# Kernel optimization log

Hardware: AMD Instinct MI355X
Metric: run time of the kernel (lower is better)

The kernel has to match this reference:

```python
import jax, jax.numpy as jnp
import numpy as np
import math

MAXL = 3
TAUS = [16, 16, 16, 16]
OUT_TAUS = [16, 16, 16, 16]
BM_CNT = 1.0
BM_EPS = 1e-5

# (l1, l2, l) triples in the kernel's triple-loop order, bucketed by output l
TRIPLES = {l: [] for l in range(MAXL + 1)}
for _l1 in range(MAXL + 1):
    for _l2 in range(_l1 + 1):
        for _l in range(_l1 - _l2, min(_l1 + _l2, MAXL) + 1):
            TRIPLES[_l].append((_l1, _l2))

MIDDLE_TAUS = [sum(TAUS[a] * TAUS[b] for (a, b) in TRIPLES[l]) for l in range(MAXL + 1)]


def _cg_coef(l1, m1, l2, m2, l, m):
    if m1 + m2 != m:
        return 0.0
    f = math.factorial
    pre = math.sqrt((2 * l + 1) * f(l1 + l2 - l) * f(l1 - l2 + l) * f(-l1 + l2 + l) / f(l1 + l2 + l + 1))
    pre *= math.sqrt(f(l + m) * f(l - m) * f(l1 - m1) * f(l1 + m1) * f(l2 - m2) * f(l2 + m2))
    s = 0.0
    for k in range(0, l1 + l2 - l + 1):
        d = [k, l1 + l2 - l - k, l1 - m1 - k, l2 + m2 - k, l - l2 + m1 + k, l - l1 - m2 + k]
        if any(x < 0 for x in d):
            continue
        den = 1.0
        for x in d:
            den *= f(x)
        s += (-1.0) ** k / den
    return pre * s


def _cg_tensor(l1, l2, l):
    t = np.zeros((2 * l1 + 1, 2 * l2 + 1, 2 * l + 1), dtype=np.float32)
    for i, m1 in enumerate(range(-l1, l1 + 1)):
        for j, m2 in enumerate(range(-l2, l2 + 1)):
            m = m1 + m2
            if -l <= m <= l:
                t[i, j, m + l] = _cg_coef(l1, m1, l2, m2, l, m)
    return t

CG = {}
for _l in range(MAXL + 1):
    for (_l1, _l2) in TRIPLES[_l]:
        CG[(_l1, _l2, _l)] = jnp.asarray(_cg_tensor(_l1, _l2, _l))

# complex-multiply contraction tensor: (a*b)[k] = a[i] b[j] CM[i,j,k]
_CM = np.zeros((2, 2, 2), dtype=np.float32)
_CM[0, 0, 0] = 1.0; _CM[1, 1, 0] = -1.0; _CM[0, 1, 1] = 1.0; _CM[1, 0, 1] = 1.0
CM = jnp.asarray(_CM)


def setup_inputs() -> dict:
    key = jax.random.key(0)
    k1, k2, k3 = jax.random.split(key, 3)
    in_len = sum(TAUS[l] * (2 * l + 1) for l in range(MAXL + 1))  # 256
    wlen = sum(OUT_TAUS[l] * MIDDLE_TAUS[l] for l in range(MAXL + 1))  # 90112
    activations = jax.random.normal(k1, (2048, in_len, 2), dtype=jnp.float32)
    W = 0.05 * jax.random.uniform(k2, (wlen, 2), dtype=jnp.float32)
    bn_stds = jax.random.uniform(k3, (sum(MIDDLE_TAUS),), dtype=jnp.float32)
    return {"activations": activations, "W": W, "bn_stds": bn_stds}


def reference(activations, W, bn_stds):
    B = activations.shape[0]
    # split input into per-l parts: [B, tau_l, 2l+1, 2]
    Fs = []
    st = 0
    for l in range(MAXL + 1):
        ln = TAUS[l] * (2 * l + 1)
        Fs.append(activations[:, st:st + ln, :].reshape(B, TAUS[l], 2 * l + 1, 2))
        st += ln
    outs = []
    w_st = 0
    s_st = 0
    for l in range(MAXL + 1):
        # Clebsch-Gordan products feeding output degree l
        mids = []
        for (l1, l2) in TRIPLES[l]:
            c = jnp.einsum('btmi,bsnj,mnp,ijk->btspk', Fs[l1], Fs[l2], CG[(l1, l2, l)], CM)
            mids.append(c.reshape(B, TAUS[l1] * TAUS[l2], 2 * l + 1, 2))
        mid = jnp.concatenate(mids, axis=1)  # [B, M_l, 2l+1, 2]
        Ml = MIDDLE_TAUS[l]
        # fused batchnorm: per-middle-channel std over batch and m, moving average update
        batch_std = jnp.sqrt(jnp.mean(jnp.sum(mid * mid, axis=-1), axis=(0, 2)))  # [M_l]
        mov = bn_stds[s_st:s_st + Ml]
        new_std = (mov * BM_CNT + batch_std) / (BM_CNT + 1.0)
        mid = mid / (new_std + BM_EPS)[None, :, None, None]
        # complex linear mix over middle channels -> out_taus[l]
        wl = jax.lax.dynamic_slice_in_dim(W, w_st, OUT_TAUS[l] * Ml, axis=0).reshape(OUT_TAUS[l], Ml, 2)
        out_l = jnp.einsum('oci,bcmj,ijk->bomk', wl, mid, CM)
        outs.append(out_l.reshape(B, OUT_TAUS[l] * (2 * l + 1), 2))
        w_st += OUT_TAUS[l] * Ml
        s_st += Ml
    return jnp.concatenate(outs, axis=1)  # [B, 256, 2]
```

## Files before the change

### kernel.cpp

```cpp
#include <hip/hip_runtime.h>
#include <math.h>

typedef __attribute__((ext_vector_type(8))) short bf16x8;
typedef __attribute__((ext_vector_type(4))) float f32x4;

constexpr double cfact(int n){ double r=1.0; for(int i=2;i<=n;++i) r*=(double)i; return r; }
constexpr double csqrt_(double x){ double g=(x>1.0)?x:1.0; for(int i=0;i<100;++i) g=0.5*(g+x/g); return g; }
constexpr double cg_coef_(int l1,int m1,int l2,int m2,int l,int m){
  double pre = csqrt_((double)(2*l+1)*cfact(l1+l2-l)*cfact(l1-l2+l)*cfact(-l1+l2+l)/cfact(l1+l2+l+1));
  pre = pre*csqrt_(cfact(l+m)*cfact(l-m)*cfact(l1-m1)*cfact(l1+m1)*cfact(l2-m2)*cfact(l2+m2));
  double s=0.0;
  for(int k=0;k<=l1+l2-l;++k){
    int d0=k,d1=l1+l2-l-k,d2=l1-m1-k,d3=l2+m2-k,d4=l-l2+m1+k,d5=l-l1-m2+k;
    if(d0<0||d1<0||d2<0||d3<0||d4<0||d5<0) continue;
    double den=cfact(d0)*cfact(d1)*cfact(d2)*cfact(d3)*cfact(d4)*cfact(d5);
    s+=((k&1)?-1.0:1.0)/den;
  }
  return pre*s;
}
struct CGList{ int n; float coef[64]; int mi[64]; int ni[64]; int pi[64]; };
constexpr CGList build_cg(int l1,int l2,int l){
  CGList T{};
  for(int i=0;i<2*l1+1;++i){
    for(int j=0;j<2*l2+1;++j){
      int m1=i-l1, m2=j-l2, m=m1+m2;
      if(m<-l||m>l) continue;
      double c=cg_coef_(l1,m1,l2,m2,l,m);
      if(c>1e-12||c<-1e-12){
        T.coef[T.n]=(float)c; T.mi[T.n]=i; T.ni[T.n]=j; T.pi[T.n]=m+l; T.n++;
      }
    }
  }
  return T;
}

__device__ __host__ constexpr int AOFF(int l){ return l==0?0: l==1?16: l==2?64:144; }
__device__ __host__ constexpr int MLs(int l){ return l==0?1024: l==1?1536: l==2?1792:1536; }
__device__ __host__ constexpr int WOFF(int l){ return l==0?0: l==1?16384: l==2?40960:69632; }
__device__ __host__ constexpr int SOFF(int l){ return l==0?0: l==1?1024: l==2?2560:4352; }
__device__ __host__ constexpr int NTRI(int l){ return l==0?4: l==1?6: l==2?7:6; }
__device__ __host__ constexpr int ABASE(int l){ return l==0?0: l==1?65536: l==2?163840:278528; }
__device__ __host__ constexpr size_t MBW(int l){ return l==0?0 : l==1?2097152 : l==2?11534336 : 29884416; }
#define MID_OFF 1048576
#define MID_BYTES ((size_t)51904512*4)

#define DEVFN __device__ __forceinline__
#define LPITCH 144
#define APITCH 132

DEVFN unsigned f2bf2(float x, float y){
  unsigned ux = __float_as_uint(x); ux = (ux + 0x7FFFu + ((ux>>16)&1u)) >> 16;
  unsigned uy = __float_as_uint(y); uy = (uy + 0x7FFFu + ((uy>>16)&1u)) >> 16;
  return (ux & 0xFFFFu) | (uy << 16);
}

template<int L1,int L2,int L>
DEVFN void cg_accum(const float2* F1, const float2* F2, float2* mid){
  constexpr CGList T = build_cg(L1,L2,L);
  #pragma unroll
  for(int e=0;e<T.n;++e){
    const float c = T.coef[e];
    const float2 a = F1[T.mi[e]];
    const float2 b = F2[T.ni[e]];
    float pr = a.x*b.x - a.y*b.y;
    float pim= a.x*b.y + a.y*b.x;
    mid[T.pi[e]].x += c*pr;
    mid[T.pi[e]].y += c*pim;
  }
}

template<int L1,int L2,int L,int Q>
DEVFN void k1_body(const float2* __restrict__ acts, int b0, int u, int bh,
                   float& ssa, float& ssb, unsigned* __restrict__ midw){
  constexpr int N1=2*L1+1, N2=2*L2+1, NP=2*L+1, Ml=MLs(L);
  const int t = u>>3, s0 = (u&7)*2;
  unsigned* midq = midw ? (midw + MBW(L) + (size_t)Q*256) : nullptr;
  #pragma unroll 2
  for(int bi=0;bi<8;++bi){
    const int row = bh*8 + bi;
    const float2* arow = acts + row*256;
    float2 F1[N1], F2a[N2], F2b[N2], mida[NP], midb[NP];
    #pragma unroll
    for(int m=0;m<N1;++m) F1[m]=arow[AOFF(L1)+t*N1+m];
    #pragma unroll
    for(int n=0;n<N2;++n){
      F2a[n]=arow[AOFF(L2)+s0*N2+n];
      F2b[n]=arow[AOFF(L2)+(s0+1)*N2+n];
    }
    #pragma unroll
    for(int p=0;p<NP;++p){ mida[p]=make_float2(0.f,0.f); midb[p]=make_float2(0.f,0.f); }
    cg_accum<L1,L2,L>(F1,F2a,mida);
    cg_accum<L1,L2,L>(F1,F2b,midb);
    #pragma unroll
    for(int p=0;p<NP;++p){
      ssa += mida[p].x*mida[p].x + mida[p].y*mida[p].y;
      ssb += midb[p].x*midb[p].x + midb[p].y*midb[p].y;
    }
    if(midq){
      const size_t nrow = (size_t)(b0+row)*NP;
      #pragma unroll
      for(int p=0;p<NP;++p){
        uint2 v; v.x = f2bf2(mida[p].x, mida[p].y); v.y = f2bf2(midb[p].x, midb[p].y);
        ((uint2*)(midq + (nrow+p)*Ml))[u] = v;
      }
    }
  }
}

__global__ __launch_bounds__(256) void k_sumsq(const float* __restrict__ act,
                                               float* __restrict__ sumsq,
                                               unsigned* __restrict__ midw){
  __shared__ float2 acts[16*256];
  int bid=blockIdx.x;
  const int order[23] = {22,16,21,18,15,20,13,9,14,8,17,7,12,6,10,3,5,19,2,11,1,4,0};
  int ti = order[bid>>7];
  int b0 = (bid&127)*16;
  const int tid = threadIdx.x;
  {
    const float4* ag = (const float4*)act + (size_t)b0*128;
    float4* as4 = (float4*)acts;
    #pragma unroll
    for(int j=0;j<8;++j) as4[j*256+tid] = ag[j*256+tid];
  }
  __syncthreads();
  const int u = tid & 127, bh = tid >> 7;
  float ssa=0.f, ssb=0.f;
  switch(ti){
    case 0:  k1_body<0,0,0,0>(acts,b0,u,bh,ssa,ssb,midw); break;
    case 1:  k1_body<1,1,0,1>(acts,b0,u,bh,ssa,ssb,midw); break;
    case 2:  k1_body<2,2,0,2>(acts,b0,u,bh,ssa,ssb,midw); break;
    case 3:  k1_body<3,3,0,3>(acts,b0,u,bh,ssa,ssb,midw); break;
    case 4:  k1_body<1,0,1,0>(acts,b0,u,bh,ssa,ssb,midw); break;
    case 5:  k1_body<1,1,1,1>(acts,b0,u,bh,ssa,ssb,midw); break;
    case 6:  k1_body<2,1,1,2>(acts,b0,u,bh,ssa,ssb,midw); break;
    case 7:  k1_body<2,2,1,3>(acts,b0,u,bh,ssa,ssb,midw); break;
    case 8:  k1_body<3,2,1,4>(acts,b0,u,bh,ssa,ssb,midw); break;
    case 9:  k1_body<3,3,1,5>(acts,b0,u,bh,ssa,ssb,midw); break;
    case 10: k1_body<1,1,2,0>(acts,b0,u,bh,ssa,ssb,midw); break;
    case 11: k1_body<2,0,2,1>(acts,b0,u,bh,ssa,ssb,midw); break;
    case 12: k1_body<2,1,2,2>(acts,b0,u,bh,ssa,ssb,midw); break;
    case 13: k1_body<2,2,2,3>(acts,b0,u,bh,ssa,ssb,midw); break;
    case 14: k1_body<3,1,2,4>(acts,b0,u,bh,ssa,ssb,midw); break;
    case 15: k1_body<3,2,2,5>(acts,b0,u,bh,ssa,ssb,midw); break;
    case 16: k1_body<3,3,2,6>(acts,b0,u,bh,ssa,ssb,midw); break;
    case 17: k1_body<2,1,3,0>(acts,b0,u,bh,ssa,ssb,midw); break;
    case 18: k1_body<2,2,3,1>(acts,b0,u,bh,ssa,ssb,midw); break;
    case 19: k1_body<3,0,3,2>(acts,b0,u,bh,ssa,ssb,midw); break;
    case 20: k1_body<3,1,3,3>(acts,b0,u,bh,ssa,ssb,midw); break;
    case 21: k1_body<3,2,3,4>(acts,b0,u,bh,ssa,ssb,midw); break;
    default: k1_body<3,3,3,5>(acts,b0,u,bh,ssa,ssb,midw); break;
  }
  atomicAdd(&sumsq[ti*256 + 2*u],     ssa);
  atomicAdd(&sumsq[ti*256 + 2*u + 1], ssb);
}

__global__ __launch_bounds__(256) void k_buildA(const float* __restrict__ W,
                                                const float* __restrict__ bn,
                                                const float* __restrict__ sumsq,
                                                short* __restrict__ A){
  int idx = blockIdx.x*256 + threadIdx.x;
  if(idx>=5888) return;
  int l = (idx<1024)?0 : (idx<2560)?1 : (idx<4352)?2 : 3;
  float divi = (l==0)?(1.f/2048.f) : (l==1)?(1.f/6144.f) : (l==2)?(1.f/10240.f) : (1.f/14336.f);
  float bstd = sqrtf(sumsq[idx]*divi);
  float nstd = 0.5f*(bn[idx]+bstd);
  float s = 1.f/(nstd+1e-5f);
  int c = idx - SOFF(l);
  int Ml = MLs(l);
  const float2* wbase = (const float2*)W + WOFF(l) + c;
  unsigned* Aw = (unsigned*)(A + ABASE(l));
  for(int o=0;o<16;++o){
    float2 w = wbase[(size_t)o*Ml];
    Aw[(size_t)o*Ml + c]      = f2bf2(w.x*s, -w.y*s);
    Aw[(size_t)(o+16)*Ml + c] = f2bf2(w.y*s,  w.x*s);
  }
}

template<int L>
DEVFN void k4_panel(int tg, const unsigned* __restrict__ midl,
                    const short* __restrict__ A_l, float* __restrict__ out,
                    unsigned* ldsA){
  constexpr int NP = 2*L+1;
  constexpr int Ml = MLs(L);
  constexpr int NK = Ml/16;
  constexpr int P  = NK/8;
  const int tid = threadIdx.x;
  const int lane = tid & 63, w = tid >> 6;
  const int col = lane & 15, quad = lane >> 4;
  const int nt = tg*8 + w;
  const unsigned* Aw = (const unsigned*)A_l;
  const unsigned* bp = midl + (size_t)(nt*16 + col)*Ml + quad*4;

  const int r0 = tid >> 5,        j0 = (tid & 31)*4;
  const int r1 = (tid+512) >> 5,  j1 = j0;

  f32x4 cR = {0.f,0.f,0.f,0.f};
  f32x4 cI = {0.f,0.f,0.f,0.f};
  {
    uint4 v0 = *(const uint4*)(Aw + (size_t)r0*Ml + j0);
    uint4 v1 = *(const uint4*)(Aw + (size_t)r1*Ml + j1);
    *(uint4*)(ldsA + r0*APITCH + j0) = v0;
    *(uint4*)(ldsA + r1*APITCH + j1) = v1;
  }
  __syncthreads();
  for(int p=0; p<P; ++p){
    const unsigned* buf  = ldsA + (p&1)*(32*APITCH);
    unsigned* nbuf = ldsA + ((p+1)&1)*(32*APITCH);
    uint4 v0, v1;
    if(p+1 < P){
      v0 = *(const uint4*)(Aw + (size_t)r0*Ml + (p+1)*128 + j0);
      v1 = *(const uint4*)(Aw + (size_t)r1*Ml + (p+1)*128 + j1);
    }
    const unsigned* bpp = bp + p*128;
    const unsigned* a0 = buf + col*APITCH + quad*4;
    const unsigned* a1 = buf + (col+16)*APITCH + quad*4;
    #pragma unroll
    for(int c=0; c<8; ++c){
      bf16x8 b  = *(const bf16x8*)(bpp + c*16);
      bf16x8 A0 = *(const bf16x8*)(a0 + c*16);
      bf16x8 A1 = *(const bf16x8*)(a1 + c*16);
      cR = __builtin_amdgcn_mfma_f32_16x16x32_bf16(A0, b, cR, 0, 0, 0);
      cI = __builtin_amdgcn_mfma_f32_16x16x32_bf16(A1, b, cI, 0, 0, 0);
    }
    if(p+1 < P){
      *(uint4*)(nbuf + r0*APITCH + j0) = v0;
      *(uint4*)(nbuf + r1*APITCH + j1) = v1;
    }
    __syncthreads();
  }
  const int n = nt*16 + col;
  const int b = n / NP, pp = n % NP;
  float2* out2 = (float2*)out;
  #pragma unroll
  for(int i=0;i<4;++i){
    const int o = quad*4 + i;
    out2[(size_t)b*256 + AOFF(L) + o*NP + pp] = make_float2(cR[i], cI[i]);
  }
}

__global__ __launch_bounds__(512) void k_gemm4(const unsigned* __restrict__ midw,
                                               const short* __restrict__ A,
                                               float* __restrict__ out){
  __shared__ unsigned ldsA[2*32*APITCH];
  const int bid = blockIdx.x;
  if(bid < 16)       k4_panel<0>(bid,       midw+MBW(0), A+ABASE(0), out, ldsA);
  else if(bid < 64)  k4_panel<1>(bid - 16,  midw+MBW(1), A+ABASE(1), out, ldsA);
  else if(bid < 144) k4_panel<2>(bid - 64,  midw+MBW(2), A+ABASE(2), out, ldsA);
  else               k4_panel<3>(bid - 144, midw+MBW(3), A+ABASE(3), out, ldsA);
}

template<int L1,int L2,int L>
DEVFN void phase1(const float2* __restrict__ act2, unsigned* ldsw,
                  int half, int c0, int bh4, int b_lo, int b_hi, int n0){
  constexpr int N1=2*L1+1, N2=2*L2+1, NP=2*L+1;
  const int s  = c0 & 15;
  const int t1 = half*8 + (c0>>4);
  const int t2 = t1 + 4;
  for(int b = b_lo + bh4; b <= b_hi; b += 4){
    const float2* arow = act2 + (size_t)b*256;
    float2 F1a[N1], F1b[N1], F2[N2], mida[NP], midb[NP];
    #pragma unroll
    for(int m=0;m<N1;++m){
      F1a[m]=arow[AOFF(L1)+t1*N1+m];
      F1b[m]=arow[AOFF(L1)+t2*N1+m];
    }
    #pragma unroll
    for(int n=0;n<N2;++n) F2[n]=arow[AOFF(L2)+s*N2+n];
    #pragma unroll
    for(int p=0;p<NP;++p){ mida[p]=make_float2(0.f,0.f); midb[p]=make_float2(0.f,0.f); }
    cg_accum<L1,L2,L>(F1a,F2,mida);
    cg_accum<L1,L2,L>(F1b,F2,midb);
    int nb = b*NP - n0;
    #pragma unroll
    for(int p=0;p<NP;++p){
      int n = nb + p;
      if(n>=0 && n<32){
        ldsw[n*LPITCH + c0]      = f2bf2(mida[p].x, mida[p].y);
        ldsw[n*LPITCH + c0 + 64] = f2bf2(midb[p].x, midb[p].y);
      }
    }
  }
}

template<int L>
DEVFN void p1_dispatch(int q, int half, const float2* __restrict__ act2, unsigned* ldsw,
                       int c0,int bh4,int b_lo,int b_hi,int n0){
  if constexpr(L==0){
    switch(q){
      case 0: phase1<0,0,0>(act2,ldsw,half,c0,bh4,b_lo,b_hi,n0); break;
      case 1: phase1<1,1,0>(act2,ldsw,half,c0,bh4,b_lo,b_hi,n0); break;
      case 2: phase1<2,2,0>(act2,ldsw,half,c0,bh4,b_lo,b_hi,n0); break;
      default:phase1<3,3,0>(act2,ldsw,half,c0,bh4,b_lo,b_hi,n0); break;
    }
  } else if constexpr(L==1){
    switch(q){
      case 0: phase1<1,0,1>(act2,ldsw,half,c0,bh4,b_lo,b_hi,n0); break;
      case 1: phase1<1,1,1>(act2,ldsw,half,c0,bh4,b_lo,b_hi,n0); break;
      case 2: phase1<2,1,1>(act2,ldsw,half,c0,bh4,b_lo,b_hi,n0); break;
      case 3: phase1<2,2,1>(act2,ldsw,half,c0,bh4,b_lo,b_hi,n0); break;
      case 4: phase1<3,2,1>(act2,ldsw,half,c0,bh4,b_lo,b_hi,n0); break;
      default:phase1<3,3,1>(act2,ldsw,half,c0,bh4,b_lo,b_hi,n0); break;
    }
  } else if constexpr(L==2){
    switch(q){
      case 0: phase1<1,1,2>(act2,ldsw,half,c0,bh4,b_lo,b_hi,n0); break;
      case 1: phase1<2,0,2>(act2,ldsw,half,c0,bh4,b_lo,b_hi,n0); break;
      case 2: phase1<2,1,2>(act2,ldsw,half,c0,bh4,b_lo,b_hi,n0); break;
      case 3: phase1<2,2,2>(act2,ldsw,half,c0,bh4,b_lo,b_hi,n0); break;
      case 4: phase1<3,1,2>(act2,ldsw,half,c0,bh4,b_lo,b_hi,n0); break;
      case 5: phase1<3,2,2>(act2,ldsw,half,c0,bh4,b_lo,b_hi,n0); break;
      default:phase1<3,3,2>(act2,ldsw,half,c0,bh4,b_lo,b_hi,n0); break;
    }
  } else {
    switch(q){
      case 0: phase1<2,1,3>(act2,ldsw,half,c0,bh4,b_lo,b_hi,n0); break;
      case 1: phase1<2,2,3>(act2,ldsw,half,c0,bh4,b_lo,b_hi,n0); break;
      case 2: phase1<3,0,3>(act2,ldsw,half,c0,bh4,b_lo,b_hi,n0); break;
      case 3: phase1<3,1,3>(act2,ldsw,half,c0,bh4,b_lo,b_hi,n0); break;
      case 4: phase1<3,2,3>(act2,ldsw,half,c0,bh4,b_lo,b_hi,n0); break;
      default:phase1<3,3,3>(act2,ldsw,half,c0,bh4,b_lo,b_hi,n0); break;
    }
  }
}

template<int L>
DEVFN void k3_gemm(int n0, const float2* __restrict__ act2,
                   const short* __restrict__ A_l, float* __restrict__ out,
                   unsigned* lds){
  constexpr int NP = 2*L+1;
  constexpr int NT = NTRI(L);
  constexpr int pitchA = 2*MLs(L);
  const int tid = threadIdx.x;
  const int lane = tid & 63, wsub = tid >> 6;
  const int col = lane & 15, quad = lane >> 4;
  const int nh = wsub & 1, mh = wsub >> 1;
  const int c0 = tid & 63, bh4 = tid >> 6;
  const int b_lo = n0 / NP;
  const int b_hi = (n0 + 31) / NP;

  f32x4 acc = {0.f,0.f,0.f,0.f};
  const short* Ar = A_l + (size_t)(col + mh*16) * pitchA + quad*8;
  const int lds_rd = (nh*16 + col)*LPITCH + quad*4;

  for(int chunk = 0; chunk < 2*NT; ++chunk){
    const int q = chunk >> 1, half = chunk & 1;
    unsigned* buf = lds + (chunk & 1)*(32*LPITCH);
    p1_dispatch<L>(q, half, act2, buf, c0, bh4, b_lo, b_hi, n0);
    __syncthreads();
    const int kbase = q*512 + half*256;
    const char* ldsb = (const char*)(buf + lds_rd);
    #pragma unroll
    for(int ks=0; ks<8; ++ks){
      bf16x8 a = *(const bf16x8*)(Ar + kbase + ks*32);
      bf16x8 b = *(const bf16x8*)(ldsb + ks*64);
      acc = __builtin_amdgcn_mfma_f32_16x16x32_bf16(a, b, acc, 0, 0, 0);
    }
  }
  const int n = n0 + nh*16 + col;
  const int b = n / NP, p = n % NP;
  #pragma unroll
  for(int i=0;i<4;++i){
    const int o = quad*4 + i;
    out[((size_t)b*256 + AOFF(L) + o*NP + p)*2 + mh] = acc[i];
  }
}

__global__ __launch_bounds__(256) void k_gemm(const float* __restrict__ act,
                                              const short* __restrict__ A,
                                              float* __restrict__ out){
  __shared__ unsigned lds[2*32*LPITCH];
  const int bid = blockIdx.x;
  const float2* act2 = (const float2*)act;
  if(bid < 64)       k3_gemm<0>((bid      )*32, act2, A + ABASE(0), out, lds);
  else if(bid < 256) k3_gemm<1>((bid - 64 )*32, act2, A + ABASE(1), out, lds);
  else if(bid < 576) k3_gemm<2>((bid - 256)*32, act2, A + ABASE(2), out, lds);
  else               k3_gemm<3>((bid - 576)*32, act2, A + ABASE(3), out, lds);
}

extern "C" void kernel_launch(void* const* d_in, const int* in_sizes, int n_in,
                              void* d_out, int out_size, void* d_ws, size_t ws_size,
                              hipStream_t stream) {
  const float* act = (const float*)d_in[0];
  const float* W   = (const float*)d_in[1];
  const float* bn  = (const float*)d_in[2];
  float* out = (float*)d_out;

  float* sumsq = (float*)d_ws;
  short* A     = (short*)((char*)d_ws + 24576);
  const size_t REQ = (size_t)MID_OFF + MID_BYTES;
  unsigned* midw = (ws_size >= REQ) ? (unsigned*)((char*)d_ws + MID_OFF) : nullptr;

  hipMemsetAsync(sumsq, 0, 5888*sizeof(float), stream);
  hipLaunchKernelGGL(k_sumsq,  dim3(23*128), dim3(256), 0, stream, act, sumsq, midw);
  hipLaunchKernelGGL(k_buildA, dim3(23),     dim3(256), 0, stream, W, bn, sumsq, A);
  if(midw)
    hipLaunchKernelGGL(k_gemm4, dim3(256),  dim3(512), 0, stream, (const unsigned*)midw, A, out);
  else
    hipLaunchKernelGGL(k_gemm,  dim3(1024), dim3(256), 0, stream, act, A, out);
}
```

Baseline: 166.5 us.

## Register-prefetch B panels in GEMM, halve block size, use nontemporal mid stores

The final GEMM kernel now runs 256-thread blocks with 4 waves each, so there are twice as many blocks covering the same tiles. It double-buffers the bf16 middle-activation B operand in registers via nontemporal loads, one K-panel ahead, on top of the existing LDS double-buffer for A. The sumsq kernel now writes the intermediate mid tensor with nontemporal 64-bit stores to limit cache pollution. The aim is to hide global-load latency of the streamed B operand and improve occupancy and load balance. The costs are higher register pressure from holding 16 bf16x8 vectors, and the A panel is now reloaded by more blocks.

```diff
diff --git a/kernel.cpp b/kernel.cpp
--- a/kernel.cpp
+++ b/kernel.cpp
@@ -100,8 +100,10 @@
       const size_t nrow = (size_t)(b0+row)*NP;
       #pragma unroll
       for(int p=0;p<NP;++p){
-        uint2 v; v.x = f2bf2(mida[p].x, mida[p].y); v.y = f2bf2(midb[p].x, midb[p].y);
-        ((uint2*)(midq + (nrow+p)*Ml))[u] = v;
+        unsigned lo = f2bf2(mida[p].x, mida[p].y);
+        unsigned hi = f2bf2(midb[p].x, midb[p].y);
+        unsigned long long pv = (unsigned long long)lo | ((unsigned long long)hi<<32);
+        __builtin_nontemporal_store(pv, (unsigned long long*)(midq + (nrow+p)*Ml) + u);
       }
     }
   }
@@ -177,7 +179,7 @@
 }
 
 template<int L>
-DEVFN void k4_panel(int tg, const unsigned* __restrict__ midl,
+DEVFN void k5_panel(int tg, const unsigned* __restrict__ midl,
                     const short* __restrict__ A_l, float* __restrict__ out,
                     unsigned* ldsA){
   constexpr int NP = 2*L+1;
@@ -187,44 +189,57 @@
   const int tid = threadIdx.x;
   const int lane = tid & 63, w = tid >> 6;
   const int col = lane & 15, quad = lane >> 4;
-  const int nt = tg*8 + w;
+  const int nt = tg*4 + w;
   const unsigned* Aw = (const unsigned*)A_l;
   const unsigned* bp = midl + (size_t)(nt*16 + col)*Ml + quad*4;
 
-  const int r0 = tid >> 5,        j0 = (tid & 31)*4;
-  const int r1 = (tid+512) >> 5,  j1 = j0;
-
   f32x4 cR = {0.f,0.f,0.f,0.f};
   f32x4 cI = {0.f,0.f,0.f,0.f};
-  {
-    uint4 v0 = *(const uint4*)(Aw + (size_t)r0*Ml + j0);
-    uint4 v1 = *(const uint4*)(Aw + (size_t)r1*Ml + j1);
-    *(uint4*)(ldsA + r0*APITCH + j0) = v0;
-    *(uint4*)(ldsA + r1*APITCH + j1) = v1;
-  }
+
+  #pragma unroll
+  for(int sub=0;sub<4;++sub){
+    int idx = sub*256 + tid, r = idx>>5, j = (idx&31)*4;
+    *(uint4*)(ldsA + r*APITCH + j) = *(const uint4*)(Aw + (size_t)r*Ml + j);
+  }
+  bf16x8 b0[8], b1[8];
+  #pragma unroll
+  for(int c=0;c<8;++c) b0[c] = __builtin_nontemporal_load((const bf16x8*)(bp + c*16));
   __syncthreads();
-  for(int p=0; p<P; ++p){
-    const unsigned* buf  = ldsA + (p&1)*(32*APITCH);
-    unsigned* nbuf = ldsA + ((p+1)&1)*(32*APITCH);
-    uint4 v0, v1;
+
+  #pragma unroll
+  for(int p=0;p<P;++p){
+    bf16x8* bc = (p&1)? b1 : b0;
+    bf16x8* bn = (p&1)? b0 : b1;
     if(p+1 < P){
-      v0 = *(const uint4*)(Aw + (size_t)r0*Ml + (p+1)*128 + j0);
-      v1 = *(const uint4*)(Aw + (size_t)r1*Ml + (p+1)*128 + j1);
-    }
-    const unsigned* bpp = bp + p*128;
+      #pragma unroll
+      for(int c=0;c<8;++c)
+        bn[c] = __builtin_nontemporal_load((const bf16x8*)(bp + (p+1)*128 + c*16));
+    }
+    uint4 v[4];
+    if(p+1 < P){
+      #pragma unroll
+      for(int sub=0;sub<4;++sub){
+        int idx = sub*256 + tid, r = idx>>5, j = (idx&31)*4;
+        v[sub] = *(const uint4*)(Aw + (size_t)r*Ml + (p+1)*128 + j);
+      }
+    }
+    const unsigned* buf = ldsA + (p&1)*(32*APITCH);
     const unsigned* a0 = buf + col*APITCH + quad*4;
     const unsigned* a1 = buf + (col+16)*APITCH + quad*4;
     #pragma unroll
-    for(int c=0; c<8; ++c){
-      bf16x8 b  = *(const bf16x8*)(bpp + c*16);
+    for(int c=0;c<8;++c){
       bf16x8 A0 = *(const bf16x8*)(a0 + c*16);
       bf16x8 A1 = *(const bf16x8*)(a1 + c*16);
-      cR = __builtin_amdgcn_mfma_f32_16x16x32_bf16(A0, b, cR, 0, 0, 0);
-      cI = __builtin_amdgcn_mfma_f32_16x16x32_bf16(A1, b, cI, 0, 0, 0);
+      cR = __builtin_amdgcn_mfma_f32_16x16x32_bf16(A0, bc[c], cR, 0, 0, 0);
+      cI = __builtin_amdgcn_mfma_f32_16x16x32_bf16(A1, bc[c], cI, 0, 0, 0);
     }
     if(p+1 < P){
-      *(uint4*)(nbuf + r0*APITCH + j0) = v0;
-      *(uint4*)(nbuf + r1*APITCH + j1) = v1;
+      unsigned* nbuf = ldsA + ((p+1)&1)*(32*APITCH);
+      #pragma unroll
+      for(int sub=0;sub<4;++sub){
+        int idx = sub*256 + tid, r = idx>>5, j = (idx&31)*4;
+        *(uint4*)(nbuf + r*APITCH + j) = v[sub];
+      }
     }
     __syncthreads();
   }
@@ -238,15 +253,15 @@
   }
 }
 
-__global__ __launch_bounds__(512) void k_gemm4(const unsigned* __restrict__ midw,
+__global__ __launch_bounds__(256) void k_gemm5(const unsigned* __restrict__ midw,
                                                const short* __restrict__ A,
                                                float* __restrict__ out){
   __shared__ unsigned ldsA[2*32*APITCH];
   const int bid = blockIdx.x;
-  if(bid < 16)       k4_panel<0>(bid,       midw+MBW(0), A+ABASE(0), out, ldsA);
-  else if(bid < 64)  k4_panel<1>(bid - 16,  midw+MBW(1), A+ABASE(1), out, ldsA);
-  else if(bid < 144) k4_panel<2>(bid - 64,  midw+MBW(2), A+ABASE(2), out, ldsA);
-  else               k4_panel<3>(bid - 144, midw+MBW(3), A+ABASE(3), out, ldsA);
+  if(bid < 32)       k5_panel<0>(bid,       midw+MBW(0), A+ABASE(0), out, ldsA);
+  else if(bid < 128) k5_panel<1>(bid - 32,  midw+MBW(1), A+ABASE(1), out, ldsA);
+  else if(bid < 288) k5_panel<2>(bid - 128, midw+MBW(2), A+ABASE(2), out, ldsA);
+  else               k5_panel<3>(bid - 288, midw+MBW(3), A+ABASE(3), out, ldsA);
 }
 
 template<int L1,int L2,int L>
@@ -394,7 +409,7 @@
   hipLaunchKernelGGL(k_sumsq,  dim3(23*128), dim3(256), 0, stream, act, sumsq, midw);
   hipLaunchKernelGGL(k_buildA, dim3(23),     dim3(256), 0, stream, W, bn, sumsq, A);
   if(midw)
-    hipLaunchKernelGGL(k_gemm4, dim3(256),  dim3(512), 0, stream, (const unsigned*)midw, A, out);
+    hipLaunchKernelGGL(k_gemm5, dim3(512),  dim3(256), 0, stream, (const unsigned*)midw, A, out);
   else
     hipLaunchKernelGGL(k_gemm,  dim3(1024), dim3(256), 0, stream, act, A, out);
 }
```

Measured after the change: 185.6 us. +11.4%, slower.

## Exploit l1==l2 pair symmetry to shrink the mid tensor and GEMM K dimension

Applied to the files above, without the earlier changes.

For CG triples with l1==l2, the products for (t,s) and (s,t) are related by a sign of (-1)^l. The change stores only the upper-triangular channel pairs and folds the mirrored weights and batchnorm scales into the A matrix. This shrinks the bf16 intermediate written to and read from global memory, and shortens the reduction dimension of the MFMA GEMM. Mid writes become nontemporal stores. The fallback path that recomputes products inside the GEMM is removed, so the workspace must now be large enough. An extra memset zeroes the padded A, and the last K chunk is clamped for padding.

```diff
diff --git a/kernel.cpp b/kernel.cpp
--- a/kernel.cpp
+++ b/kernel.cpp
@@ -38,14 +38,17 @@
 __device__ __host__ constexpr int MLs(int l){ return l==0?1024: l==1?1536: l==2?1792:1536; }
 __device__ __host__ constexpr int WOFF(int l){ return l==0?0: l==1?16384: l==2?40960:69632; }
 __device__ __host__ constexpr int SOFF(int l){ return l==0?0: l==1?1024: l==2?2560:4352; }
-__device__ __host__ constexpr int NTRI(int l){ return l==0?4: l==1?6: l==2?7:6; }
-__device__ __host__ constexpr int ABASE(int l){ return l==0?0: l==1?65536: l==2?163840:278528; }
-__device__ __host__ constexpr size_t MBW(int l){ return l==0?0 : l==1?2097152 : l==2?11534336 : 29884416; }
+__device__ __host__ constexpr int MLP_(int l){ return l==0?544: l==1?1184: l==2?1440:1296; }
+__device__ __host__ constexpr size_t MBW(int l){ return l==0?0 : l==1?1114112 : l==2?8388608 : 23134208; }
 #define MID_OFF 1048576
-#define MID_BYTES ((size_t)51904512*4)
+#define MID_BYTES ((size_t)41713664*4)
+__device__ __host__ constexpr int PAW(int l){ return l==0?640: l==1?1280: l==2?1536:1408; }
+__device__ __host__ constexpr int ABW(int l){ return l==0?0: l==1?20480: l==2?61440:110592; }
+#define A_WORDS 155648
+__device__ __host__ constexpr int NKc(int l){ return MLP_(l)/16; }
+__device__ __host__ constexpr int PNc(int l){ return (NKc(l)+7)/8; }
 
 #define DEVFN __device__ __forceinline__
-#define LPITCH 144
 #define APITCH 132
 
 DEVFN unsigned f2bf2(float x, float y){
@@ -69,12 +72,19 @@
   }
 }
 
-template<int L1,int L2,int L,int Q>
+template<int L1,int L2,int L,int PB>
 DEVFN void k1_body(const float2* __restrict__ acts, int b0, int u, int bh,
                    float& ssa, float& ssb, unsigned* __restrict__ midw){
-  constexpr int N1=2*L1+1, N2=2*L2+1, NP=2*L+1, Ml=MLs(L);
+  constexpr int N1=2*L1+1, N2=2*L2+1, NP=2*L+1, MLP=MLP_(L);
+  constexpr bool SYM = (L1==L2);
   const int t = u>>3, s0 = (u&7)*2;
-  unsigned* midq = midw ? (midw + MBW(L) + (size_t)Q*256) : nullptr;
+  unsigned* midl = midw + MBW(L);
+  int offA, offB; bool wA, wB;
+  if constexpr (SYM){
+    const int base = PB + t*16 + s0 - ((t*(t+1))>>1);
+    offA = base; offB = base+1;
+    wA = (t<=s0); wB = (t<=s0+1);
+  } else { offA = PB + 2*u; offB = offA+1; wA = true; wB = true; }
   #pragma unroll 2
   for(int bi=0;bi<8;++bi){
     const int row = bh*8 + bi;
@@ -96,12 +106,19 @@
       ssa += mida[p].x*mida[p].x + mida[p].y*mida[p].y;
       ssb += midb[p].x*midb[p].x + midb[p].y*midb[p].y;
     }
-    if(midq){
-      const size_t nrow = (size_t)(b0+row)*NP;
+    {
+      const size_t nbase = (size_t)(b0+row)*NP;
       #pragma unroll
       for(int p=0;p<NP;++p){
-        uint2 v; v.x = f2bf2(mida[p].x, mida[p].y); v.y = f2bf2(midb[p].x, midb[p].y);
-        ((uint2*)(midq + (nrow+p)*Ml))[u] = v;
+        unsigned* rp = midl + (nbase+p)*MLP;
+        if constexpr (SYM){
+          if(wA) __builtin_nontemporal_store(f2bf2(mida[p].x,mida[p].y), rp+offA);
+          if(wB) __builtin_nontemporal_store(f2bf2(midb[p].x,midb[p].y), rp+offB);
+        } else {
+          unsigned long long pv = (unsigned long long)f2bf2(mida[p].x,mida[p].y)
+                                | ((unsigned long long)f2bf2(midb[p].x,midb[p].y)<<32);
+          __builtin_nontemporal_store(pv, (unsigned long long*)(rp+offA));
+        }
       }
     }
   }
@@ -126,29 +143,29 @@
   const int u = tid & 127, bh = tid >> 7;
   float ssa=0.f, ssb=0.f;
   switch(ti){
-    case 0:  k1_body<0,0,0,0>(acts,b0,u,bh,ssa,ssb,midw); break;
-    case 1:  k1_body<1,1,0,1>(acts,b0,u,bh,ssa,ssb,midw); break;
-    case 2:  k1_body<2,2,0,2>(acts,b0,u,bh,ssa,ssb,midw); break;
-    case 3:  k1_body<3,3,0,3>(acts,b0,u,bh,ssa,ssb,midw); break;
-    case 4:  k1_body<1,0,1,0>(acts,b0,u,bh,ssa,ssb,midw); break;
-    case 5:  k1_body<1,1,1,1>(acts,b0,u,bh,ssa,ssb,midw); break;
-    case 6:  k1_body<2,1,1,2>(acts,b0,u,bh,ssa,ssb,midw); break;
-    case 7:  k1_body<2,2,1,3>(acts,b0,u,bh,ssa,ssb,midw); break;
-    case 8:  k1_body<3,2,1,4>(acts,b0,u,bh,ssa,ssb,midw); break;
-    case 9:  k1_body<3,3,1,5>(acts,b0,u,bh,ssa,ssb,midw); break;
-    case 10: k1_body<1,1,2,0>(acts,b0,u,bh,ssa,ssb,midw); break;
-    case 11: k1_body<2,0,2,1>(acts,b0,u,bh,ssa,ssb,midw); break;
-    case 12: k1_body<2,1,2,2>(acts,b0,u,bh,ssa,ssb,midw); break;
-    case 13: k1_body<2,2,2,3>(acts,b0,u,bh,ssa,ssb,midw); break;
-    case 14: k1_body<3,1,2,4>(acts,b0,u,bh,ssa,ssb,midw); break;
-    case 15: k1_body<3,2,2,5>(acts,b0,u,bh,ssa,ssb,midw); break;
-    case 16: k1_body<3,3,2,6>(acts,b0,u,bh,ssa,ssb,midw); break;
-    case 17: k1_body<2,1,3,0>(acts,b0,u,bh,ssa,ssb,midw); break;
-    case 18: k1_body<2,2,3,1>(acts,b0,u,bh,ssa,ssb,midw); break;
-    case 19: k1_body<3,0,3,2>(acts,b0,u,bh,ssa,ssb,midw); break;
-    case 20: k1_body<3,1,3,3>(acts,b0,u,bh,ssa,ssb,midw); break;
-    case 21: k1_body<3,2,3,4>(acts,b0,u,bh,ssa,ssb,midw); break;
-    default: k1_body<3,3,3,5>(acts,b0,u,bh,ssa,ssb,midw); break;
+    case 0:  k1_body<0,0,0,0>   (acts,b0,u,bh,ssa,ssb,midw); break;
+    case 1:  k1_body<1,1,0,136> (acts,b0,u,bh,ssa,ssb,midw); break;
+    case 2:  k1_body<2,2,0,272> (acts,b0,u,bh,ssa,ssb,midw); break;
+    case 3:  k1_body<3,3,0,408> (acts,b0,u,bh,ssa,ssb,midw); break;
+    case 4:  k1_body<1,0,1,0>   (acts,b0,u,bh,ssa,ssb,midw); break;
+    case 5:  k1_body<1,1,1,256> (acts,b0,u,bh,ssa,ssb,midw); break;
+    case 6:  k1_body<2,1,1,392> (acts,b0,u,bh,ssa,ssb,midw); break;
+    case 7:  k1_body<2,2,1,648> (acts,b0,u,bh,ssa,ssb,midw); break;
+    case 8:  k1_body<3,2,1,784> (acts,b0,u,bh,ssa,ssb,midw); break;
+    case 9:  k1_body<3,3,1,1040>(acts,b0,u,bh,ssa,ssb,midw); break;
+    case 10: k1_body<1,1,2,0>   (acts,b0,u,bh,ssa,ssb,midw); break;
+    case 11: k1_body<2,0,2,136> (acts,b0,u,bh,ssa,ssb,midw); break;
+    case 12: k1_body<2,1,2,392> (acts,b0,u,bh,ssa,ssb,midw); break;
+    case 13: k1_body<2,2,2,648> (acts,b0,u,bh,ssa,ssb,midw); break;
+    case 14: k1_body<3,1,2,784> (acts,b0,u,bh,ssa,ssb,midw); break;
+    case 15: k1_body<3,2,2,1040>(acts,b0,u,bh,ssa,ssb,midw); break;
+    case 16: k1_body<3,3,2,1296>(acts,b0,u,bh,ssa,ssb,midw); break;
+    case 17: k1_body<2,1,3,0>   (acts,b0,u,bh,ssa,ssb,midw); break;
+    case 18: k1_body<2,2,3,256> (acts,b0,u,bh,ssa,ssb,midw); break;
+    case 19: k1_body<3,0,3,392> (acts,b0,u,bh,ssa,ssb,midw); break;
+    case 20: k1_body<3,1,3,648> (acts,b0,u,bh,ssa,ssb,midw); break;
+    case 21: k1_body<3,2,3,904> (acts,b0,u,bh,ssa,ssb,midw); break;
+    default: k1_body<3,3,3,1160>(acts,b0,u,bh,ssa,ssb,midw); break;
   }
   atomicAdd(&sumsq[ti*256 + 2*u],     ssa);
   atomicAdd(&sumsq[ti*256 + 2*u + 1], ssb);
@@ -157,74 +174,85 @@
 __global__ __launch_bounds__(256) void k_buildA(const float* __restrict__ W,
                                                 const float* __restrict__ bn,
                                                 const float* __restrict__ sumsq,
-                                                short* __restrict__ A){
+                                                unsigned* __restrict__ A){
   int idx = blockIdx.x*256 + threadIdx.x;
   if(idx>=5888) return;
   int l = (idx<1024)?0 : (idx<2560)?1 : (idx<4352)?2 : 3;
+  int c = idx - SOFF(l);
+  int q = c>>8, cc = c&255, t = cc>>4, ss = cc&15;
+  const unsigned char symf[4][7] = {{1,1,1,1,0,0,0},{0,1,0,1,0,1,0},
+                                    {1,0,0,1,0,0,1},{0,1,0,0,0,1,0}};
+  const short pbt[4][7] = {{0,136,272,408,0,0,0},{0,256,392,648,784,1040,0},
+                           {0,136,392,648,784,1040,1296},{0,256,392,648,904,1160,0}};
+  bool sym = symf[l][q];
+  if(sym && t>ss) return;
   float divi = (l==0)?(1.f/2048.f) : (l==1)?(1.f/6144.f) : (l==2)?(1.f/10240.f) : (1.f/14336.f);
-  float bstd = sqrtf(sumsq[idx]*divi);
-  float nstd = 0.5f*(bn[idx]+bstd);
-  float s = 1.f/(nstd+1e-5f);
-  int c = idx - SOFF(l);
+  float s1 = 1.f/(0.5f*(bn[idx]+sqrtf(sumsq[idx]*divi))+1e-5f);
   int Ml = MLs(l);
-  const float2* wbase = (const float2*)W + WOFF(l) + c;
-  unsigned* Aw = (unsigned*)(A + ABASE(l));
+  const float2* w1 = (const float2*)W + WOFF(l) + c;
+  const float2* w2 = nullptr; float s2 = 0.f;
+  if(sym && t<ss){
+    int c2 = q*256 + ss*16 + t;
+    int i2 = SOFF(l) + c2;
+    float sg = (l&1)? -1.f : 1.f;
+    s2 = sg/(0.5f*(bn[i2]+sqrtf(sumsq[i2]*divi))+1e-5f);
+    w2 = (const float2*)W + WOFF(l) + c2;
+  }
+  int pc = sym ? (pbt[l][q] + t*16+ss - ((t*(t+1))>>1)) : (pbt[l][q] + cc);
+  unsigned* Aw = A + ABW(l);
+  const int PA = PAW(l);
   for(int o=0;o<16;++o){
-    float2 w = wbase[(size_t)o*Ml];
-    Aw[(size_t)o*Ml + c]      = f2bf2(w.x*s, -w.y*s);
-    Aw[(size_t)(o+16)*Ml + c] = f2bf2(w.y*s,  w.x*s);
+    float2 w = w1[(size_t)o*Ml];
+    float wex = w.x*s1, wey = w.y*s1;
+    if(w2){ float2 v = w2[(size_t)o*Ml]; wex += v.x*s2; wey += v.y*s2; }
+    Aw[(size_t)o*PA + pc]      = f2bf2(wex, -wey);
+    Aw[(size_t)(o+16)*PA + pc] = f2bf2(wey,  wex);
   }
 }
 
 template<int L>
-DEVFN void k4_panel(int tg, const unsigned* __restrict__ midl,
-                    const short* __restrict__ A_l, float* __restrict__ out,
+DEVFN void k6_panel(int tg, const unsigned* __restrict__ midl,
+                    const unsigned* __restrict__ Aw, float* __restrict__ out,
                     unsigned* ldsA){
-  constexpr int NP = 2*L+1;
-  constexpr int Ml = MLs(L);
-  constexpr int NK = Ml/16;
-  constexpr int P  = NK/8;
+  constexpr int NP = 2*L+1, MLP = MLP_(L), NK = NKc(L), PN = PNc(L), PA = PAW(L);
   const int tid = threadIdx.x;
   const int lane = tid & 63, w = tid >> 6;
   const int col = lane & 15, quad = lane >> 4;
   const int nt = tg*8 + w;
-  const unsigned* Aw = (const unsigned*)A_l;
-  const unsigned* bp = midl + (size_t)(nt*16 + col)*Ml + quad*4;
-
-  const int r0 = tid >> 5,        j0 = (tid & 31)*4;
-  const int r1 = (tid+512) >> 5,  j1 = j0;
+  const unsigned* bp = midl + (size_t)(nt*16 + col)*MLP + quad*4;
+  const int r0 = tid >> 5, j0 = (tid & 31)*4, r1 = (tid+512) >> 5;
 
   f32x4 cR = {0.f,0.f,0.f,0.f};
   f32x4 cI = {0.f,0.f,0.f,0.f};
   {
-    uint4 v0 = *(const uint4*)(Aw + (size_t)r0*Ml + j0);
-    uint4 v1 = *(const uint4*)(Aw + (size_t)r1*Ml + j1);
+    uint4 v0 = *(const uint4*)(Aw + (size_t)r0*PA + j0);
+    uint4 v1 = *(const uint4*)(Aw + (size_t)r1*PA + j0);
     *(uint4*)(ldsA + r0*APITCH + j0) = v0;
-    *(uint4*)(ldsA + r1*APITCH + j1) = v1;
+    *(uint4*)(ldsA + r1*APITCH + j0) = v1;
   }
   __syncthreads();
-  for(int p=0; p<P; ++p){
+  for(int p=0; p<PN; ++p){
     const unsigned* buf  = ldsA + (p&1)*(32*APITCH);
     unsigned* nbuf = ldsA + ((p+1)&1)*(32*APITCH);
     uint4 v0, v1;
-    if(p+1 < P){
-      v0 = *(const uint4*)(Aw + (size_t)r0*Ml + (p+1)*128 + j0);
-      v1 = *(const uint4*)(Aw + (size_t)r1*Ml + (p+1)*128 + j1);
-    }
-    const unsigned* bpp = bp + p*128;
+    if(p+1 < PN){
+      v0 = *(const uint4*)(Aw + (size_t)r0*PA + (p+1)*128 + j0);
+      v1 = *(const uint4*)(Aw + (size_t)r1*PA + (p+1)*128 + j0);
+    }
     const unsigned* a0 = buf + col*APITCH + quad*4;
     const unsigned* a1 = buf + (col+16)*APITCH + quad*4;
     #pragma unroll
     for(int c=0; c<8; ++c){
-      bf16x8 b  = *(const bf16x8*)(bpp + c*16);
+      int kc = p*8 + c; kc = (kc > NK-1) ? NK-1 : kc;
+      bf16x8 b  = *(const bf16x8*)(bp + (size_t)kc*16);
       bf16x8 A0 = *(const bf16x8*)(a0 + c*16);
       bf16x8 A1 = *(const bf16x8*)(a1 + c*16);
       cR = __builtin_amdgcn_mfma_f32_16x16x32_bf16(A0, b, cR, 0, 0, 0);
       cI = __builtin_amdgcn_mfma_f32_16x16x32_bf16(A1, b, cI, 0, 0, 0);
     }
-    if(p+1 < P){
+    if(p+1 < PN){
       *(uint4*)(nbuf + r0*APITCH + j0) = v0;
-      *(uint4*)(nbuf + r1*APITCH + j1) = v1;
+      *(uint4*)(nbuf + r1*APITCH + j0) = v1;
     }
     __syncthreads();
   }
@@ -238,143 +266,15 @@
   }
 }
 
-__global__ __launch_bounds__(512) void k_gemm4(const unsigned* __restrict__ midw,
-                                               const short* __restrict__ A,
+__global__ __launch_bounds__(512) void k_gemm6(const unsigned* __restrict__ midw,
+                                               const unsigned* __restrict__ A,
                                                float* __restrict__ out){
   __shared__ unsigned ldsA[2*32*APITCH];
   const int bid = blockIdx.x;
-  if(bid < 16)       k4_panel<0>(bid,       midw+MBW(0), A+ABASE(0), out, ldsA);
-  else if(bid < 64)  k4_panel<1>(bid - 16,  midw+MBW(1), A+ABASE(1), out, ldsA);
-  else if(bid < 144) k4_panel<2>(bid - 64,  midw+MBW(2), A+ABASE(2), out, ldsA);
-  else               k4_panel<3>(bid - 144, midw+MBW(3), A+ABASE(3), out, ldsA);
-}
-
-template<int L1,int L2,int L>
-DEVFN void phase1(const float2* __restrict__ act2, unsigned* ldsw,
-                  int half, int c0, int bh4, int b_lo, int b_hi, int n0){
-  constexpr int N1=2*L1+1, N2=2*L2+1, NP=2*L+1;
-  const int s  = c0 & 15;
-  const int t1 = half*8 + (c0>>4);
-  const int t2 = t1 + 4;
-  for(int b = b_lo + bh4; b <= b_hi; b += 4){
-    const float2* arow = act2 + (size_t)b*256;
-    float2 F1a[N1], F1b[N1], F2[N2], mida[NP], midb[NP];
-    #pragma unroll
-    for(int m=0;m<N1;++m){
-      F1a[m]=arow[AOFF(L1)+t1*N1+m];
-      F1b[m]=arow[AOFF(L1)+t2*N1+m];
-    }
-    #pragma unroll
-    for(int n=0;n<N2;++n) F2[n]=arow[AOFF(L2)+s*N2+n];
-    #pragma unroll
-    for(int p=0;p<NP;++p){ mida[p]=make_float2(0.f,0.f); midb[p]=make_float2(0.f,0.f); }
-    cg_accum<L1,L2,L>(F1a,F2,mida);
-    cg_accum<L1,L2,L>(F1b,F2,midb);
-    int nb = b*NP - n0;
-    #pragma unroll
-    for(int p=0;p<NP;++p){
-      int n = nb + p;
-      if(n>=0 && n<32){
-        ldsw[n*LPITCH + c0]      = f2bf2(mida[p].x, mida[p].y);
-        ldsw[n*LPITCH + c0 + 64] = f2bf2(midb[p].x, midb[p].y);
-      }
-    }
-  }
-}
-
-template<int L>
-DEVFN void p1_dispatch(int q, int half, const float2* __restrict__ act2, unsigned* ldsw,
-                       int c0,int bh4,int b_lo,int b_hi,int n0){
-  if constexpr(L==0){
-    switch(q){
-      case 0: phase1<0,0,0>(act2,ldsw,half,c0,bh4,b_lo,b_hi,n0); break;
-      case 1: phase1<1,1,0>(act2,ldsw,half,c0,bh4,b_lo,b_hi,n0); break;
-      case 2: phase1<2,2,0>(act2,ldsw,half,c0,bh4,b_lo,b_hi,n0); break;
-      default:phase1<3,3,0>(act2,ldsw,half,c0,bh4,b_lo,b_hi,n0); break;
-    }
-  } else if constexpr(L==1){
-    switch(q){
-      case 0: phase1<1,0,1>(act2,ldsw,half,c0,bh4,b_lo,b_hi,n0); break;
-      case 1: phase1<1,1,1>(act2,ldsw,half,c0,bh4,b_lo,b_hi,n0); break;
-      case 2: phase1<2,1,1>(act2,ldsw,half,c0,bh4,b_lo,b_hi,n0); break;
-      case 3: phase1<2,2,1>(act2,ldsw,half,c0,bh4,b_lo,b_hi,n0); break;
-      case 4: phase1<3,2,1>(act2,ldsw,half,c0,bh4,b_lo,b_hi,n0); break;
-      default:phase1<3,3,1>(act2,ldsw,half,c0,bh4,b_lo,b_hi,n0); break;
-    }
-  } else if constexpr(L==2){
-    switch(q){
-      case 0: phase1<1,1,2>(act2,ldsw,half,c0,bh4,b_lo,b_hi,n0); break;
-      case 1: phase1<2,0,2>(act2,ldsw,half,c0,bh4,b_lo,b_hi,n0); break;
-      case 2: phase1<2,1,2>(act2,ldsw,half,c0,bh4,b_lo,b_hi,n0); break;
-      case 3: phase1<2,2,2>(act2,ldsw,half,c0,bh4,b_lo,b_hi,n0); break;
-      case 4: phase1<3,1,2>(act2,ldsw,half,c0,bh4,b_lo,b_hi,n0); break;
-      case 5: phase1<3,2,2>(act2,ldsw,half,c0,bh4,b_lo,b_hi,n0); break;
-      default:phase1<3,3,2>(act2,ldsw,half,c0,bh4,b_lo,b_hi,n0); break;
-    }
-  } else {
-    switch(q){
-      case 0: phase1<2,1,3>(act2,ldsw,half,c0,bh4,b_lo,b_hi,n0); break;
-      case 1: phase1<2,2,3>(act2,ldsw,half,c0,bh4,b_lo,b_hi,n0); break;
-      case 2: phase1<3,0,3>(act2,ldsw,half,c0,bh4,b_lo,b_hi,n0); break;
-      case 3: phase1<3,1,3>(act2,ldsw,half,c0,bh4,b_lo,b_hi,n0); break;
-      case 4: phase1<3,2,3>(act2,ldsw,half,c0,bh4,b_lo,b_hi,n0); break;
-      default:phase1<3,3,3>(act2,ldsw,half,c0,bh4,b_lo,b_hi,n0); break;
-    }
-  }
-}
-
-template<int L>
-DEVFN void k3_gemm(int n0, const float2* __restrict__ act2,
-                   const short* __restrict__ A_l, float* __restrict__ out,
-                   unsigned* lds){
-  constexpr int NP = 2*L+1;
-  constexpr int NT = NTRI(L);
-  constexpr int pitchA = 2*MLs(L);
-  const int tid = threadIdx.x;
-  const int lane = tid & 63, wsub = tid >> 6;
-  const int col = lane & 15, quad = lane >> 4;
-  const int nh = wsub & 1, mh = wsub >> 1;
-  const int c0 = tid & 63, bh4 = tid >> 6;
-  const int b_lo = n0 / NP;
-  const int b_hi = (n0 + 31) / NP;
-
-  f32x4 acc = {0.f,0.f,0.f,0.f};
-  const short* Ar = A_l + (size_t)(col + mh*16) * pitchA + quad*8;
-  const int lds_rd = (nh*16 + col)*LPITCH + quad*4;
-
-  for(int chunk = 0; chunk < 2*NT; ++chunk){
-    const int q = chunk >> 1, half = chunk & 1;
-    unsigned* buf = lds + (chunk & 1)*(32*LPITCH);
-    p1_dispatch<L>(q, half, act2, buf, c0, bh4, b_lo, b_hi, n0);
-    __syncthreads();
-    const int kbase = q*512 + half*256;
-    const char* ldsb = (const char*)(buf + lds_rd);
-    #pragma unroll
-    for(int ks=0; ks<8; ++ks){
-      bf16x8 a = *(const bf16x8*)(Ar + kbase + ks*32);
-      bf16x8 b = *(const bf16x8*)(ldsb + ks*64);
-      acc = __builtin_amdgcn_mfma_f32_16x16x32_bf16(a, b, acc, 0, 0, 0);
-    }
-  }
-  const int n = n0 + nh*16 + col;
-  const int b = n / NP, p = n % NP;
-  #pragma unroll
-  for(int i=0;i<4;++i){
-    const int o = quad*4 + i;
-    out[((size_t)b*256 + AOFF(L) + o*NP + p)*2 + mh] = acc[i];
-  }
-}
-
-__global__ __launch_bounds__(256) void k_gemm(const float* __restrict__ act,
-                                              const short* __restrict__ A,
-                                              float* __restrict__ out){
-  __shared__ unsigned lds[2*32*LPITCH];
-  const int bid = blockIdx.x;
-  const float2* act2 = (const float2*)act;
-  if(bid < 64)       k3_gemm<0>((bid      )*32, act2, A + ABASE(0), out, lds);
-  else if(bid < 256) k3_gemm<1>((bid - 64 )*32, act2, A + ABASE(1), out, lds);
-  else if(bid < 576) k3_gemm<2>((bid - 256)*32, act2, A + ABASE(2), out, lds);
-  else               k3_gemm<3>((bid - 576)*32, act2, A + ABASE(3), out, lds);
+  if(bid < 16)       k6_panel<0>(bid,       midw+MBW(0), A+ABW(0), out, ldsA);
+  else if(bid < 64)  k6_panel<1>(bid - 16,  midw+MBW(1), A+ABW(1), out, ldsA);
+  else if(bid < 144) k6_panel<2>(bid - 64,  midw+MBW(2), A+ABW(2), out, ldsA);
+  else               k6_panel<3>(bid - 144, midw+MBW(3), A+ABW(3), out, ldsA);
 }
 
 extern "C" void kernel_launch(void* const* d_in, const int* in_sizes, int n_in,
@@ -385,16 +285,13 @@
   const float* bn  = (const float*)d_in[2];
   float* out = (float*)d_out;
 
-  float* sumsq = (float*)d_ws;
-  short* A     = (short*)((char*)d_ws + 24576);
-  const size_t REQ = (size_t)MID_OFF + MID_BYTES;
-  unsigned* midw = (ws_size >= REQ) ? (unsigned*)((char*)d_ws + MID_OFF) : nullptr;
+  float*    sumsq = (float*)d_ws;
+  unsigned* A     = (unsigned*)((char*)d_ws + 24576);
+  unsigned* midw  = (unsigned*)((char*)d_ws + MID_OFF);
 
   hipMemsetAsync(sumsq, 0, 5888*sizeof(float), stream);
+  hipMemsetAsync(A, 0, A_WORDS*sizeof(unsigned), stream);
   hipLaunchKernelGGL(k_sumsq,  dim3(23*128), dim3(256), 0, stream, act, sumsq, midw);
   hipLaunchKernelGGL(k_buildA, dim3(23),     dim3(256), 0, stream, W, bn, sumsq, A);
-  if(midw)
-    hipLaunchKernelGGL(k_gemm4, dim3(256),  dim3(512), 0, stream, (const unsigned*)midw, A, out);
-  else
-    hipLaunchKernelGGL(k_gemm,  dim3(1024), dim3(256), 0, stream, act, A, out);
-}
+  hipLaunchKernelGGL(k_gemm6,  dim3(256),    dim3(512), 0, stream, midw, A, out);
+}
```

After: 179.7 us. +7.9%, slower.
